# Optimization experiments

Hardware: AMD Instinct MI355X
Metric: run time of the kernel (lower is better)

## Reference

```python
import jax, jax.numpy as jnp
import numpy as np

N_NODES = 50000
N_EDGES = 800000
IN_CH = 128
OUT_CH = 64
HID = 2 * OUT_CH  # 128
NEG_SLOPE = 0.2  # PyG GATConv default negative_slope


def gat_conv(x, edge_index, W, a_src, a_dst, b):
    """Single-head PyG GATConv (heads=1, concat=True, self-loops already in edge_index)."""
    N = x.shape[0]
    h = x @ W  # [N, C]
    src, dst = edge_index[0], edge_index[1]
    # per-edge attention logits: leaky_relu(a_src . h_src + a_dst . h_dst)
    e = jax.nn.leaky_relu((h @ a_src)[src] + (h @ a_dst)[dst], NEG_SLOPE)  # [E]
    # softmax over incoming edges of each dst node (numerically stable)
    m = jax.ops.segment_max(e, dst, num_segments=N)
    p = jnp.exp(e - m[dst])
    denom = jax.ops.segment_sum(p, dst, num_segments=N)
    coef = p / denom[dst]  # [E]
    # scatter-aggregate weighted source features
    out = jax.ops.segment_sum(coef[:, None] * h[src], dst, num_segments=N)  # [N, C]
    return out + b


def setup_inputs() -> dict:
    key = jax.random.key(0)
    ks = jax.random.split(key, 12)
    s_in = 1.0 / np.sqrt(IN_CH)
    s_h = 1.0 / np.sqrt(HID)
    return {
        "x": jax.random.normal(ks[0], (N_NODES, IN_CH), dtype=jnp.float32),
        "edge_index": jax.random.randint(ks[1], (2, N_EDGES), 0, N_NODES, dtype=jnp.int64),
        "W1": jax.random.normal(ks[2], (IN_CH, HID), dtype=jnp.float32) * s_in,
        "a_src1": jax.random.normal(ks[3], (HID,), dtype=jnp.float32) * s_h,
        "a_dst1": jax.random.normal(ks[4], (HID,), dtype=jnp.float32) * s_h,
        "b1": jnp.zeros((HID,), dtype=jnp.float32),
        "W_mu": jax.random.normal(ks[5], (HID, OUT_CH), dtype=jnp.float32) * s_h,
        "a_src_mu": jax.random.normal(ks[6], (OUT_CH,), dtype=jnp.float32) * 0.125,
        "a_dst_mu": jax.random.normal(ks[7], (OUT_CH,), dtype=jnp.float32) * 0.125,
        "b_mu": jnp.zeros((OUT_CH,), dtype=jnp.float32),
        "W_ls": jax.random.normal(ks[8], (HID, OUT_CH), dtype=jnp.float32) * s_h,
        "a_src_ls": jax.random.normal(ks[9], (OUT_CH,), dtype=jnp.float32) * 0.125,
        "a_dst_ls": jax.random.normal(ks[10], (OUT_CH,), dtype=jnp.float32) * 0.125,
        "b_ls": jnp.zeros((OUT_CH,), dtype=jnp.float32),
    }


def reference(x, edge_index, W1, a_src1, a_dst1, b1, W_mu, a_src_mu, a_dst_mu, b_mu, W_ls, a_src_ls, a_dst_ls, b_ls):
    N = x.shape[0]
    loops = jnp.arange(N, dtype=edge_index.dtype)
    ei = jnp.concatenate([edge_index, jnp.stack([loops, loops])], axis=1)  # add self-loops
    h = jax.nn.relu(gat_conv(x, ei, W1, a_src1, a_dst1, b1))
    mu = gat_conv(h, ei, W_mu, a_src_mu, a_dst_mu, b_mu)
    logstd = gat_conv(h, ei, W_ls, a_src_ls, a_dst_ls, b_ls)
    return mu, logstd
```

## Files before the change

### kernel.cpp

```cpp
#include <hip/hip_runtime.h>
#include <hip/hip_bf16.h>
#include <math.h>

typedef __attribute__((ext_vector_type(8))) _Float16 half8;
typedef __attribute__((ext_vector_type(4))) float f32x4;


__device__ __forceinline__ float leaky02(float v) { return v > 0.0f ? v : 0.2f * v; }

__device__ __forceinline__ unsigned short f2bf(float f) {
  unsigned u = __float_as_uint(f);
  u += 0x7FFF + ((u >> 16) & 1);
  return (unsigned short)(u >> 16);
}
__device__ __forceinline__ float2 bfp(unsigned v) {
  float2 r;
  r.x = __uint_as_float(v << 16);
  r.y = __uint_as_float(v & 0xFFFF0000u);
  return r;
}


#define BSHIFT 9
#define BDSTS 512

__global__ __launch_bounds__(256) void bucket_hist_kernel(
    const int* __restrict__ ei, int* __restrict__ bcount, int E, int NBUCK) {
  __shared__ int h[128];
  if (threadIdx.x < 128) h[threadIdx.x] = 0;
  __syncthreads();
  for (int e = blockIdx.x * blockDim.x + threadIdx.x; e < E; e += gridDim.x * blockDim.x)
    atomicAdd(&h[ei[E + e] >> BSHIFT], 1);
  __syncthreads();
  if (threadIdx.x < NBUCK && h[threadIdx.x]) atomicAdd(&bcount[threadIdx.x], h[threadIdx.x]);
}

__global__ __launch_bounds__(128) void bucket_scan_kernel(
    const int* __restrict__ bcount, int* __restrict__ bstart, int* __restrict__ bcursor,
    int* __restrict__ row_start, int NBUCK, int E, int N) {
  __shared__ int lds[128];
  int t = threadIdx.x;
  int v = (t < NBUCK) ? bcount[t] : 0;
  lds[t] = v;
  __syncthreads();
#pragma unroll
  for (int off = 1; off < 128; off <<= 1) {
    int tmp = (t >= off) ? lds[t - off] : 0;
    __syncthreads();
    lds[t] += tmp;
    __syncthreads();
  }
  if (t < NBUCK) {
    int excl = lds[t] - v;
    bstart[t] = excl;
    bcursor[t] = excl;
  }
  if (t == 0) { bstart[NBUCK] = E; row_start[N] = E; }
}

#define CHUNK 4096
__global__ __launch_bounds__(256) void pair_scatter_kernel(
    const int* __restrict__ ei, int* __restrict__ bcursor, unsigned* __restrict__ pairs, int E) {
  __shared__ int h[128], base[128], cur[128];
  if (threadIdx.x < 128) { h[threadIdx.x] = 0; cur[threadIdx.x] = 0; }
  __syncthreads();
  int c0 = blockIdx.x * CHUNK;
  int c1 = min(c0 + CHUNK, E);
  for (int e = c0 + (int)threadIdx.x; e < c1; e += 256)
    atomicAdd(&h[ei[E + e] >> BSHIFT], 1);
  __syncthreads();
  if (threadIdx.x < 128 && h[threadIdx.x])
    base[threadIdx.x] = atomicAdd(&bcursor[threadIdx.x], h[threadIdx.x]);
  __syncthreads();
  for (int e = c0 + (int)threadIdx.x; e < c1; e += 256) {
    int dst = ei[E + e];
    int src = ei[e];
    int b = dst >> BSHIFT;
    int r = atomicAdd(&cur[b], 1);
    pairs[base[b] + r] = ((unsigned)src << BSHIFT) | (unsigned)(dst & (BDSTS - 1));
  }
}

__global__ __launch_bounds__(512) void fine_kernel(
    const unsigned* __restrict__ pairs, const int* __restrict__ bstart,
    int* __restrict__ row_start, int* __restrict__ esrc, int N) {
  __shared__ int h[BDSTS], sc[BDSTS], cur[BDSTS];
  int t = threadIdx.x;
  int b = blockIdx.x;
  int d0 = b << BSHIFT;
  int d1 = min(d0 + BDSTS, N);
  int beg = bstart[b], end = bstart[b + 1];
  h[t] = 0;
  __syncthreads();
  for (int i = beg + t; i < end; i += 512) atomicAdd(&h[pairs[i] & (BDSTS - 1)], 1);
  __syncthreads();
  int v = h[t];
  sc[t] = v;
  __syncthreads();
#pragma unroll
  for (int off = 1; off < BDSTS; off <<= 1) {
    int tmp = (t >= off) ? sc[t - off] : 0;
    __syncthreads();
    sc[t] += tmp;
    __syncthreads();
  }
  int excl = sc[t] - v;
  if (d0 + t < d1) row_start[d0 + t] = beg + excl;
  cur[t] = excl;
  __syncthreads();
  for (int i = beg + t; i < end; i += 512) {
    unsigned p = pairs[i];
    int r = atomicAdd(&cur[p & (BDSTS - 1)], 1);
    esrc[beg + r] = (int)(p >> BSHIFT);
  }
}


__global__ __launch_bounds__(256) void prep_w_kernel(
    const float* __restrict__ W1, const float* __restrict__ Wmu, const float* __restrict__ Wls,
    _Float16* __restrict__ Wt1, _Float16* __restrict__ Wt2) {
  int idx = blockIdx.x * 256 + threadIdx.x;
  int c = idx >> 7, k = idx & 127;
  Wt1[idx] = (_Float16)W1[k * 128 + c];
  float w2 = (c < 64) ? Wmu[k * 64 + c] : Wls[k * 64 + (c - 64)];
  Wt2[idx] = (_Float16)w2;
}


__global__ __launch_bounds__(256) void gemm1_mfma(
    const float* __restrict__ X, const _Float16* __restrict__ Wt,
    const float* __restrict__ a_src, const float* __restrict__ a_dst,
    unsigned short* __restrict__ Hb, float* __restrict__ asrc, float* __restrict__ adst, int N) {
  const int wid = threadIdx.x >> 6, lane = threadIdx.x & 63;
  const int r16 = (blockIdx.x * 4 + wid) * 16;
  if (r16 >= N) return;
  const int cg = lane & 15;
  const int kq = (lane >> 4) * 8;
  const int rA = r16 + cg;
  const int rowClamp = min(rA, N - 1);

  f32x4 acc[8];
#pragma unroll
  for (int j = 0; j < 8; ++j) acc[j] = (f32x4){0.f, 0.f, 0.f, 0.f};

#pragma unroll
  for (int ks = 0; ks < 4; ++ks) {
    const int k0 = ks * 32;
    const float* xp = X + (size_t)rowClamp * 128 + k0 + kq;
    float4 xa = *(const float4*)xp;
    float4 xb = *(const float4*)(xp + 4);
    half8 a;
    a[0] = (_Float16)xa.x; a[1] = (_Float16)xa.y; a[2] = (_Float16)xa.z; a[3] = (_Float16)xa.w;
    a[4] = (_Float16)xb.x; a[5] = (_Float16)xb.y; a[6] = (_Float16)xb.z; a[7] = (_Float16)xb.w;
#pragma unroll
    for (int j = 0; j < 8; ++j) {
      half8 b = *(const half8*)(Wt + (size_t)(16 * j + cg) * 128 + k0 + kq);
      acc[j] = __builtin_amdgcn_mfma_f32_16x16x32_f16(a, b, acc[j], 0, 0, 0);
    }
  }

  float as_[8], ds_[8];
#pragma unroll
  for (int j = 0; j < 8; ++j) { as_[j] = a_src[16 * j + cg]; ds_[j] = a_dst[16 * j + cg]; }
  const int rg = (lane >> 4) * 4;
#pragma unroll
  for (int reg = 0; reg < 4; ++reg) {
    int row = r16 + rg + reg;
    bool ok = row < N;
    float ps = 0.f, pd = 0.f;
#pragma unroll
    for (int j = 0; j < 8; ++j) {
      float v = acc[j][reg];
      if (ok) Hb[(size_t)row * 128 + 16 * j + cg] = f2bf(v);
      ps = fmaf(v, as_[j], ps);
      pd = fmaf(v, ds_[j], pd);
    }
#pragma unroll
    for (int o = 1; o < 16; o <<= 1) { ps += __shfl_xor(ps, o); pd += __shfl_xor(pd, o); }
    if (ok && cg == 0) { asrc[row] = ps; adst[row] = pd; }
  }
}

__global__ __launch_bounds__(256) void gemm2_mfma(
    const _Float16* __restrict__ Xh, const _Float16* __restrict__ Wt,
    const float* __restrict__ a_src_mu, const float* __restrict__ a_dst_mu,
    const float* __restrict__ a_src_ls, const float* __restrict__ a_dst_ls,
    unsigned short* __restrict__ Hb, float* __restrict__ as2, float* __restrict__ ad2, int N) {
  const int wid = threadIdx.x >> 6, lane = threadIdx.x & 63;
  const int r16 = (blockIdx.x * 4 + wid) * 16;
  if (r16 >= N) return;
  const int cg = lane & 15;
  const int kq = (lane >> 4) * 8;
  const int rA = r16 + cg;
  const int rowClamp = min(rA, N - 1);

  f32x4 acc[8];
#pragma unroll
  for (int j = 0; j < 8; ++j) acc[j] = (f32x4){0.f, 0.f, 0.f, 0.f};

#pragma unroll
  for (int ks = 0; ks < 4; ++ks) {
    const int k0 = ks * 32;
    half8 a = *(const half8*)(Xh + (size_t)rowClamp * 128 + k0 + kq);
#pragma unroll
    for (int j = 0; j < 8; ++j) {
      half8 b = *(const half8*)(Wt + (size_t)(16 * j + cg) * 128 + k0 + kq);
      acc[j] = __builtin_amdgcn_mfma_f32_16x16x32_f16(a, b, acc[j], 0, 0, 0);
    }
  }

  float asv[8], adv[8];
#pragma unroll
  for (int j = 0; j < 4; ++j) {
    asv[j] = a_src_mu[16 * j + cg]; adv[j] = a_dst_mu[16 * j + cg];
    asv[j + 4] = a_src_ls[16 * j + cg]; adv[j + 4] = a_dst_ls[16 * j + cg];
  }
  const int rg = (lane >> 4) * 4;
#pragma unroll
  for (int reg = 0; reg < 4; ++reg) {
    int row = r16 + rg + reg;
    bool ok = row < N;
    float psm = 0.f, pdm = 0.f, psl = 0.f, pdl = 0.f;
#pragma unroll
    for (int j = 0; j < 8; ++j) {
      float v = acc[j][reg];
      if (ok) Hb[(size_t)row * 128 + 16 * j + cg] = f2bf(v);
      if (j < 4) { psm = fmaf(v, asv[j], psm); pdm = fmaf(v, adv[j], pdm); }
      else       { psl = fmaf(v, asv[j], psl); pdl = fmaf(v, adv[j], pdl); }
    }
#pragma unroll
    for (int o = 1; o < 16; o <<= 1) {
      psm += __shfl_xor(psm, o); pdm += __shfl_xor(pdm, o);
      psl += __shfl_xor(psl, o); pdl += __shfl_xor(pdl, o);
    }
    if (ok && cg == 0) {
      as2[2 * row] = psm; ad2[2 * row] = pdm;
      as2[2 * row + 1] = psl; ad2[2 * row + 1] = pdl;
    }
  }
}


__global__ __launch_bounds__(256) void agg1_pv(
    const unsigned short* __restrict__ Hb, const float* __restrict__ asrc,
    const float* __restrict__ adst, const int* __restrict__ row_start,
    const int* __restrict__ esrc, const float* __restrict__ b,
    _Float16* __restrict__ hout, int N) {
  const int lane = threadIdx.x & 63;
  const int half = lane >> 5, sub = lane & 31;
  const int g = (int)(blockIdx.x * 4 + (threadIdx.x >> 6));
  const int d = g * 2 + half;
  const bool dok = d < N;
  const int dc = dok ? d : N - 1;
  const float ad = adst[dc];
  float m = leaky02(asrc[dc] + ad);
  float den = 1.0f;
  uint2 sv = *(const uint2*)(Hb + (size_t)dc * 128 + sub * 4);
  float2 f0 = bfp(sv.x), f1 = bfp(sv.y);
  float a0 = f0.x, a1 = f0.y, a2 = f1.x, a3 = f1.y;
  const int beg = row_start[dc];
  const int n = dok ? (row_start[dc + 1] - beg) : 0;
  int nmax = n;
#pragma unroll
  for (int o = 32; o > 0; o >>= 1) nmax = max(nmax, __shfl_xor(nmax, o));
  const int hbase = half * 32;
  for (int c0 = 0; c0 < nmax; c0 += 32) {
    int j = c0 + sub;
    bool v = j < n;
    int s = v ? esrc[beg + j] : dc;
    float e = v ? leaky02(asrc[s] + ad) : -INFINITY;
    float cm = e;
#pragma unroll
    for (int o = 16; o > 0; o >>= 1) cm = fmaxf(cm, __shfl_xor(cm, o));
    float mn = fmaxf(m, cm);
    float sc = __expf(m - mn);
    m = mn;
    den *= sc; a0 *= sc; a1 *= sc; a2 *= sc; a3 *= sc;
    float w = __expf(e - m);
    float ws = w;
#pragma unroll
    for (int o = 16; o > 0; o >>= 1) ws += __shfl_xor(ws, o);
    den += ws;
    int cnt = n - c0; if (cnt > 32) cnt = 32;
    int jj = 0;
    for (; jj + 4 <= cnt; jj += 4) {
      int s0 = __shfl(s, hbase + jj), s1 = __shfl(s, hbase + jj + 1);
      int s2 = __shfl(s, hbase + jj + 2), s3 = __shfl(s, hbase + jj + 3);
      float w0 = __shfl(w, hbase + jj), w1 = __shfl(w, hbase + jj + 1);
      float w2 = __shfl(w, hbase + jj + 2), w3 = __shfl(w, hbase + jj + 3);
      uint2 h0 = *(const uint2*)(Hb + (size_t)s0 * 128 + sub * 4);
      uint2 h1 = *(const uint2*)(Hb + (size_t)s1 * 128 + sub * 4);
      uint2 h2 = *(const uint2*)(Hb + (size_t)s2 * 128 + sub * 4);
      uint2 h3 = *(const uint2*)(Hb + (size_t)s3 * 128 + sub * 4);
      float2 p0 = bfp(h0.x), p1 = bfp(h0.y);
      a0 = fmaf(w0, p0.x, a0); a1 = fmaf(w0, p0.y, a1); a2 = fmaf(w0, p1.x, a2); a3 = fmaf(w0, p1.y, a3);
      p0 = bfp(h1.x); p1 = bfp(h1.y);
      a0 = fmaf(w1, p0.x, a0); a1 = fmaf(w1, p0.y, a1); a2 = fmaf(w1, p1.x, a2); a3 = fmaf(w1, p1.y, a3);
      p0 = bfp(h2.x); p1 = bfp(h2.y);
      a0 = fmaf(w2, p0.x, a0); a1 = fmaf(w2, p0.y, a1); a2 = fmaf(w2, p1.x, a2); a3 = fmaf(w2, p1.y, a3);
      p0 = bfp(h3.x); p1 = bfp(h3.y);
      a0 = fmaf(w3, p0.x, a0); a1 = fmaf(w3, p0.y, a1); a2 = fmaf(w3, p1.x, a2); a3 = fmaf(w3, p1.y, a3);
    }
    for (; jj < cnt; ++jj) {
      int sj = __shfl(s, hbase + jj);
      float wj = __shfl(w, hbase + jj);
      uint2 hv = *(const uint2*)(Hb + (size_t)sj * 128 + sub * 4);
      float2 p0 = bfp(hv.x), p1 = bfp(hv.y);
      a0 = fmaf(wj, p0.x, a0); a1 = fmaf(wj, p0.y, a1);
      a2 = fmaf(wj, p1.x, a2); a3 = fmaf(wj, p1.y, a3);
    }
  }
  if (dok) {
    float inv = 1.0f / den;
    float4 bv = *(const float4*)(b + sub * 4);
    _Float16 o4[4];
    o4[0] = (_Float16)fmaxf(fmaf(a0, inv, bv.x), 0.f);
    o4[1] = (_Float16)fmaxf(fmaf(a1, inv, bv.y), 0.f);
    o4[2] = (_Float16)fmaxf(fmaf(a2, inv, bv.z), 0.f);
    o4[3] = (_Float16)fmaxf(fmaf(a3, inv, bv.w), 0.f);
    *(uint2*)(hout + (size_t)d * 128 + sub * 4) = *(uint2*)o4;
  }
}


__global__ __launch_bounds__(256) void agg2_pv(
    const unsigned short* __restrict__ Hb,
    const float2* __restrict__ as2, const float2* __restrict__ ad2,
    const int* __restrict__ row_start, const int* __restrict__ esrc,
    const float* __restrict__ b_mu, const float* __restrict__ b_ls,
    float* __restrict__ out_mu, float* __restrict__ out_ls, int N) {
  const int lane = threadIdx.x & 63;
  const int half = lane >> 5, sub = lane & 31;
  const bool isMu = sub < 16;
  const int g = (int)(blockIdx.x * 4 + (threadIdx.x >> 6));
  const int d = g * 2 + half;
  const bool dok = d < N;
  const int dc = dok ? d : N - 1;
  const float2 adv = ad2[dc];
  const float2 asv = as2[dc];
  float mm = leaky02(asv.x + adv.x);
  float ml = leaky02(asv.y + adv.y);
  float den_m = 1.0f, den_l = 1.0f;
  uint2 sv = *(const uint2*)(Hb + (size_t)dc * 128 + sub * 4);
  float2 f0 = bfp(sv.x), f1 = bfp(sv.y);
  float a0 = f0.x, a1 = f0.y, a2 = f1.x, a3 = f1.y;
  const int beg = row_start[dc];
  const int n = dok ? (row_start[dc + 1] - beg) : 0;
  int nmax = n;
#pragma unroll
  for (int o = 32; o > 0; o >>= 1) nmax = max(nmax, __shfl_xor(nmax, o));
  const int hbase = half * 32;
  for (int c0 = 0; c0 < nmax; c0 += 32) {
    int j = c0 + sub;
    bool v = j < n;
    int s = v ? esrc[beg + j] : dc;
    float em = -INFINITY, el = -INFINITY;
    if (v) {
      float2 av = as2[s];
      em = leaky02(av.x + adv.x);
      el = leaky02(av.y + adv.y);
    }
    float cmm = em, cml = el;
#pragma unroll
    for (int o = 16; o > 0; o >>= 1) {
      cmm = fmaxf(cmm, __shfl_xor(cmm, o));
      cml = fmaxf(cml, __shfl_xor(cml, o));
    }
    float mnm = fmaxf(mm, cmm), mnl = fmaxf(ml, cml);
    float scm = __expf(mm - mnm), scl = __expf(ml - mnl);
    mm = mnm; ml = mnl;
    den_m *= scm; den_l *= scl;
    float sce = isMu ? scm : scl;
    a0 *= sce; a1 *= sce; a2 *= sce; a3 *= sce;
    float wm = __expf(em - mm), wl = __expf(el - ml);
    float wsm = wm, wsl = wl;
#pragma unroll
    for (int o = 16; o > 0; o >>= 1) {
      wsm += __shfl_xor(wsm, o);
      wsl += __shfl_xor(wsl, o);
    }
    den_m += wsm; den_l += wsl;
    int cnt = n - c0; if (cnt > 32) cnt = 32;
    int jj = 0;
    for (; jj + 4 <= cnt; jj += 4) {
      int s0 = __shfl(s, hbase + jj), s1 = __shfl(s, hbase + jj + 1);
      int s2 = __shfl(s, hbase + jj + 2), s3 = __shfl(s, hbase + jj + 3);
      float wm0 = __shfl(wm, hbase + jj), wm1 = __shfl(wm, hbase + jj + 1);
      float wm2 = __shfl(wm, hbase + jj + 2), wm3 = __shfl(wm, hbase + jj + 3);
      float wl0 = __shfl(wl, hbase + jj), wl1 = __shfl(wl, hbase + jj + 1);
      float wl2 = __shfl(wl, hbase + jj + 2), wl3 = __shfl(wl, hbase + jj + 3);
      float w0 = isMu ? wm0 : wl0, w1 = isMu ? wm1 : wl1;
      float w2 = isMu ? wm2 : wl2, w3 = isMu ? wm3 : wl3;
      uint2 h0 = *(const uint2*)(Hb + (size_t)s0 * 128 + sub * 4);
      uint2 h1 = *(const uint2*)(Hb + (size_t)s1 * 128 + sub * 4);
      uint2 h2 = *(const uint2*)(Hb + (size_t)s2 * 128 + sub * 4);
      uint2 h3 = *(const uint2*)(Hb + (size_t)s3 * 128 + sub * 4);
      float2 p0 = bfp(h0.x), p1 = bfp(h0.y);
      a0 = fmaf(w0, p0.x, a0); a1 = fmaf(w0, p0.y, a1); a2 = fmaf(w0, p1.x, a2); a3 = fmaf(w0, p1.y, a3);
      p0 = bfp(h1.x); p1 = bfp(h1.y);
      a0 = fmaf(w1, p0.x, a0); a1 = fmaf(w1, p0.y, a1); a2 = fmaf(w1, p1.x, a2); a3 = fmaf(w1, p1.y, a3);
      p0 = bfp(h2.x); p1 = bfp(h2.y);
      a0 = fmaf(w2, p0.x, a0); a1 = fmaf(w2, p0.y, a1); a2 = fmaf(w2, p1.x, a2); a3 = fmaf(w2, p1.y, a3);
      p0 = bfp(h3.x); p1 = bfp(h3.y);
      a0 = fmaf(w3, p0.x, a0); a1 = fmaf(w3, p0.y, a1); a2 = fmaf(w3, p1.x, a2); a3 = fmaf(w3, p1.y, a3);
    }
    for (; jj < cnt; ++jj) {
      int sj = __shfl(s, hbase + jj);
      float wmj = __shfl(wm, hbase + jj);
      float wlj = __shfl(wl, hbase + jj);
      float wj = isMu ? wmj : wlj;
      uint2 hv = *(const uint2*)(Hb + (size_t)sj * 128 + sub * 4);
      float2 p0 = bfp(hv.x), p1 = bfp(hv.y);
      a0 = fmaf(wj, p0.x, a0); a1 = fmaf(wj, p0.y, a1);
      a2 = fmaf(wj, p1.x, a2); a3 = fmaf(wj, p1.y, a3);
    }
  }
  if (dok) {
    float inv = isMu ? (1.0f / den_m) : (1.0f / den_l);
    const float* bp;
    float* op;
    if (isMu) { bp = b_mu + sub * 4; op = out_mu + (size_t)d * 64 + sub * 4; }
    else      { bp = b_ls + sub * 4 - 64; op = out_ls + (size_t)d * 64 + sub * 4 - 64; }
    float4 bv = *(const float4*)bp;
    float4 o;
    o.x = fmaf(a0, inv, bv.x);
    o.y = fmaf(a1, inv, bv.y);
    o.z = fmaf(a2, inv, bv.z);
    o.w = fmaf(a3, inv, bv.w);
    *(float4*)op = o;
  }
}


extern "C" void kernel_launch(void* const* d_in, const int* in_sizes, int n_in,
                              void* d_out, int out_size, void* d_ws, size_t ws_size,
                              hipStream_t stream) {
  const float* x = (const float*)d_in[0];
  const int* ei = (const int*)d_in[1];
  const float* W1 = (const float*)d_in[2];
  const float* a_src1 = (const float*)d_in[3];
  const float* a_dst1 = (const float*)d_in[4];
  const float* b1 = (const float*)d_in[5];
  const float* W_mu = (const float*)d_in[6];
  const float* a_src_mu = (const float*)d_in[7];
  const float* a_dst_mu = (const float*)d_in[8];
  const float* b_mu = (const float*)d_in[9];
  const float* W_ls = (const float*)d_in[10];
  const float* a_src_ls = (const float*)d_in[11];
  const float* a_dst_ls = (const float*)d_in[12];
  const float* b_ls = (const float*)d_in[13];

  const int N = in_sizes[0] / 128;
  const int E = in_sizes[1] / 2;
  const int NBUCK = (N + BDSTS - 1) >> BSHIFT;

  uint8_t* p = (uint8_t*)d_ws;
  auto carve = [&](size_t bytes) -> void* {
    void* q = (void*)p;
    p += (bytes + 255) & ~(size_t)255;
    return q;
  };
  int* bcount = (int*)carve((size_t)(NBUCK + 1) * 4);
  int* bstart = (int*)carve((size_t)(NBUCK + 1) * 4);
  int* bcursor = (int*)carve((size_t)NBUCK * 4);
  int* row_start = (int*)carve((size_t)(N + 1) * 4);
  int* esrc = (int*)carve((size_t)E * 4);
  unsigned* pairs = (unsigned*)carve((size_t)E * 4);
  unsigned short* Hb1 = (unsigned short*)carve((size_t)N * 128 * 2);
  _Float16* h1 = (_Float16*)carve((size_t)N * 128 * 2);
  _Float16* Wt1 = (_Float16*)carve((size_t)128 * 128 * 2);
  _Float16* Wt2 = (_Float16*)carve((size_t)128 * 128 * 2);
  float* as1 = (float*)carve((size_t)N * 4);
  float* ad1 = (float*)carve((size_t)N * 4);
  float* as2 = (float*)carve((size_t)N * 8);
  float* ad2 = (float*)carve((size_t)N * 8);

  unsigned short* Hb2 = Hb1;

  hipMemsetAsync(bcount, 0, (size_t)(NBUCK + 1) * 4, stream);
  prep_w_kernel<<<64, 256, 0, stream>>>(W1, W_mu, W_ls, Wt1, Wt2);
  bucket_hist_kernel<<<(E + 2047) / 2048, 256, 0, stream>>>(ei, bcount, E, NBUCK);
  bucket_scan_kernel<<<1, 128, 0, stream>>>(bcount, bstart, bcursor, row_start, NBUCK, E, N);
  pair_scatter_kernel<<<(E + CHUNK - 1) / CHUNK, 256, 0, stream>>>(ei, bcursor, pairs, E);
  fine_kernel<<<NBUCK, 512, 0, stream>>>(pairs, bstart, row_start, esrc, N);

  gemm1_mfma<<<(N + 63) / 64, 256, 0, stream>>>(x, Wt1, a_src1, a_dst1, Hb1, as1, ad1, N);
  const int nwaves = (N + 1) / 2;
  const int nblk = (nwaves + 3) / 4;
  agg1_pv<<<nblk, 256, 0, stream>>>(Hb1, as1, ad1, row_start, esrc, b1, h1, N);
  gemm2_mfma<<<(N + 63) / 64, 256, 0, stream>>>(h1, Wt2, a_src_mu, a_dst_mu,
                                                a_src_ls, a_dst_ls, Hb2, as2, ad2, N);
  float* out_mu = (float*)d_out;
  float* out_ls = out_mu + (size_t)N * 64;
  agg2_pv<<<nblk, 256, 0, stream>>>(Hb2, (const float2*)as2, (const float2*)ad2,
                                    row_start, esrc, b_mu, b_ls, out_mu, out_ls, N);
}
```

Measured before the change: 165.6 us.

## Drop online-max softmax, fuse bucket histogram into gemm1, shrink buckets

The aggregation kernels drop the numerically stable online-max softmax. They compute exp(leaky(e)) directly, accumulate per-lane denominators, and reduce once at the end, which removes the per-chunk max/sum shuffles and rescaling. The gather loop is unrolled to 8 edges per iteration. The bucket histogram is merged into the gemm1 launch as extra blocks, and the bucket size is halved to 256 destinations so fine_kernel runs 256-thread blocks. Skipping the max subtraction risks exp overflow for large logits, and the NBUCK buffer size must match the new bucket count (256 is needed for 50000 nodes).

```diff
diff --git a/kernel.cpp b/kernel.cpp
--- a/kernel.cpp
+++ b/kernel.cpp
@@ -21,30 +21,19 @@
 }
 
 
-#define BSHIFT 9
-#define BDSTS 512
-
-__global__ __launch_bounds__(256) void bucket_hist_kernel(
-    const int* __restrict__ ei, int* __restrict__ bcount, int E, int NBUCK) {
-  __shared__ int h[128];
-  if (threadIdx.x < 128) h[threadIdx.x] = 0;
-  __syncthreads();
-  for (int e = blockIdx.x * blockDim.x + threadIdx.x; e < E; e += gridDim.x * blockDim.x)
-    atomicAdd(&h[ei[E + e] >> BSHIFT], 1);
-  __syncthreads();
-  if (threadIdx.x < NBUCK && h[threadIdx.x]) atomicAdd(&bcount[threadIdx.x], h[threadIdx.x]);
-}
-
-__global__ __launch_bounds__(128) void bucket_scan_kernel(
+#define BSHIFT 8
+#define BDSTS 256
+
+__global__ __launch_bounds__(256) void bucket_scan_kernel(
     const int* __restrict__ bcount, int* __restrict__ bstart, int* __restrict__ bcursor,
     int* __restrict__ row_start, int NBUCK, int E, int N) {
-  __shared__ int lds[128];
+  __shared__ int lds[256];
   int t = threadIdx.x;
   int v = (t < NBUCK) ? bcount[t] : 0;
   lds[t] = v;
   __syncthreads();
 #pragma unroll
-  for (int off = 1; off < 128; off <<= 1) {
+  for (int off = 1; off < 256; off <<= 1) {
     int tmp = (t >= off) ? lds[t - off] : 0;
     __syncthreads();
     lds[t] += tmp;
@@ -61,15 +50,15 @@
 #define CHUNK 4096
 __global__ __launch_bounds__(256) void pair_scatter_kernel(
     const int* __restrict__ ei, int* __restrict__ bcursor, unsigned* __restrict__ pairs, int E) {
-  __shared__ int h[128], base[128], cur[128];
-  if (threadIdx.x < 128) { h[threadIdx.x] = 0; cur[threadIdx.x] = 0; }
+  __shared__ int h[256], base[256], cur[256];
+  h[threadIdx.x] = 0; cur[threadIdx.x] = 0;
   __syncthreads();
   int c0 = blockIdx.x * CHUNK;
   int c1 = min(c0 + CHUNK, E);
   for (int e = c0 + (int)threadIdx.x; e < c1; e += 256)
     atomicAdd(&h[ei[E + e] >> BSHIFT], 1);
   __syncthreads();
-  if (threadIdx.x < 128 && h[threadIdx.x])
+  if (h[threadIdx.x])
     base[threadIdx.x] = atomicAdd(&bcursor[threadIdx.x], h[threadIdx.x]);
   __syncthreads();
   for (int e = c0 + (int)threadIdx.x; e < c1; e += 256) {
@@ -81,18 +70,17 @@
   }
 }
 
-__global__ __launch_bounds__(512) void fine_kernel(
+__global__ __launch_bounds__(256) void fine_kernel(
     const unsigned* __restrict__ pairs, const int* __restrict__ bstart,
     int* __restrict__ row_start, int* __restrict__ esrc, int N) {
   __shared__ int h[BDSTS], sc[BDSTS], cur[BDSTS];
   int t = threadIdx.x;
   int b = blockIdx.x;
   int d0 = b << BSHIFT;
-  int d1 = min(d0 + BDSTS, N);
   int beg = bstart[b], end = bstart[b + 1];
   h[t] = 0;
   __syncthreads();
-  for (int i = beg + t; i < end; i += 512) atomicAdd(&h[pairs[i] & (BDSTS - 1)], 1);
+  for (int i = beg + t; i < end; i += 256) atomicAdd(&h[pairs[i] & (BDSTS - 1)], 1);
   __syncthreads();
   int v = h[t];
   sc[t] = v;
@@ -105,10 +93,10 @@
     __syncthreads();
   }
   int excl = sc[t] - v;
-  if (d0 + t < d1) row_start[d0 + t] = beg + excl;
+  if (d0 + t < N) row_start[d0 + t] = beg + excl;
   cur[t] = excl;
   __syncthreads();
-  for (int i = beg + t; i < end; i += 512) {
+  for (int i = beg + t; i < end; i += 256) {
     unsigned p = pairs[i];
     int r = atomicAdd(&cur[p & (BDSTS - 1)], 1);
     esrc[beg + r] = (int)(p >> BSHIFT);
@@ -127,12 +115,26 @@
 }
 
 
-__global__ __launch_bounds__(256) void gemm1_mfma(
+__global__ __launch_bounds__(256) void gemm1_hist(
     const float* __restrict__ X, const _Float16* __restrict__ Wt,
     const float* __restrict__ a_src, const float* __restrict__ a_dst,
-    unsigned short* __restrict__ Hb, float* __restrict__ asrc, float* __restrict__ adst, int N) {
+    unsigned short* __restrict__ Hb, float* __restrict__ asrc, float* __restrict__ adst, int N,
+    const int* __restrict__ ei, int* __restrict__ bcount, int E, int nGB) {
+  if ((int)blockIdx.x >= nGB) {
+    __shared__ int h[256];
+    h[threadIdx.x] = 0;
+    __syncthreads();
+    int hb = (int)blockIdx.x - nGB;
+    int c0 = hb * 2048;
+    int c1 = min(c0 + 2048, E);
+    for (int e = c0 + (int)threadIdx.x; e < c1; e += 256)
+      atomicAdd(&h[ei[E + e] >> BSHIFT], 1);
+    __syncthreads();
+    if (h[threadIdx.x]) atomicAdd(&bcount[threadIdx.x], h[threadIdx.x]);
+    return;
+  }
   const int wid = threadIdx.x >> 6, lane = threadIdx.x & 63;
-  const int r16 = (blockIdx.x * 4 + wid) * 16;
+  const int r16 = ((int)blockIdx.x * 4 + wid) * 16;
   if (r16 >= N) return;
   const int cg = lane & 15;
   const int kq = (lane >> 4) * 8;
@@ -187,7 +189,7 @@
     const float* __restrict__ a_src_ls, const float* __restrict__ a_dst_ls,
     unsigned short* __restrict__ Hb, float* __restrict__ as2, float* __restrict__ ad2, int N) {
   const int wid = threadIdx.x >> 6, lane = threadIdx.x & 63;
-  const int r16 = (blockIdx.x * 4 + wid) * 16;
+  const int r16 = ((int)blockIdx.x * 4 + wid) * 16;
   if (r16 >= N) return;
   const int cg = lane & 15;
   const int kq = (lane >> 4) * 8;
@@ -241,7 +243,17 @@
 }
 
 
-__global__ __launch_bounds__(256) void agg1_pv(
+#define GATH(K)                                                          \
+  {                                                                      \
+    int sA = __shfl(s, hbase + jj + K);                                  \
+    float wA = __shfl(w, hbase + jj + K);                                \
+    uint2 hA = *(const uint2*)(Hb + (size_t)sA * 128 + sub * 4);         \
+    float2 pa = bfp(hA.x), pb = bfp(hA.y);                               \
+    a0 = fmaf(wA, pa.x, a0); a1 = fmaf(wA, pa.y, a1);                    \
+    a2 = fmaf(wA, pb.x, a2); a3 = fmaf(wA, pb.y, a3);                    \
+  }
+
+__global__ __launch_bounds__(256) void agg1_ns(
     const unsigned short* __restrict__ Hb, const float* __restrict__ asrc,
     const float* __restrict__ adst, const int* __restrict__ row_start,
     const int* __restrict__ esrc, const float* __restrict__ b,
@@ -253,63 +265,33 @@
   const bool dok = d < N;
   const int dc = dok ? d : N - 1;
   const float ad = adst[dc];
-  float m = leaky02(asrc[dc] + ad);
-  float den = 1.0f;
+  const float wself = __expf(leaky02(asrc[dc] + ad));
   uint2 sv = *(const uint2*)(Hb + (size_t)dc * 128 + sub * 4);
   float2 f0 = bfp(sv.x), f1 = bfp(sv.y);
-  float a0 = f0.x, a1 = f0.y, a2 = f1.x, a3 = f1.y;
+  float a0 = wself * f0.x, a1 = wself * f0.y, a2 = wself * f1.x, a3 = wself * f1.y;
+  float den = (sub == 0) ? wself : 0.f;
   const int beg = row_start[dc];
   const int n = dok ? (row_start[dc + 1] - beg) : 0;
-  int nmax = n;
-#pragma unroll
-  for (int o = 32; o > 0; o >>= 1) nmax = max(nmax, __shfl_xor(nmax, o));
+  const int nmax = max(n, __shfl_xor(n, 32));
   const int hbase = half * 32;
   for (int c0 = 0; c0 < nmax; c0 += 32) {
     int j = c0 + sub;
     bool v = j < n;
-    int s = v ? esrc[beg + j] : dc;
-    float e = v ? leaky02(asrc[s] + ad) : -INFINITY;
-    float cm = e;
-#pragma unroll
-    for (int o = 16; o > 0; o >>= 1) cm = fmaxf(cm, __shfl_xor(cm, o));
-    float mn = fmaxf(m, cm);
-    float sc = __expf(m - mn);
-    m = mn;
-    den *= sc; a0 *= sc; a1 *= sc; a2 *= sc; a3 *= sc;
-    float w = __expf(e - m);
-    float ws = w;
-#pragma unroll
-    for (int o = 16; o > 0; o >>= 1) ws += __shfl_xor(ws, o);
-    den += ws;
-    int cnt = n - c0; if (cnt > 32) cnt = 32;
+    int s = v ? esrc[beg + j] : 0;
+    float w = 0.f;
+    if (v) w = __expf(leaky02(asrc[s] + ad));
+    den += w;
+    int cnt = n - c0;
+    if (cnt > 32) cnt = 32;
+    if (cnt < 0) cnt = 0;
     int jj = 0;
-    for (; jj + 4 <= cnt; jj += 4) {
-      int s0 = __shfl(s, hbase + jj), s1 = __shfl(s, hbase + jj + 1);
-      int s2 = __shfl(s, hbase + jj + 2), s3 = __shfl(s, hbase + jj + 3);
-      float w0 = __shfl(w, hbase + jj), w1 = __shfl(w, hbase + jj + 1);
-      float w2 = __shfl(w, hbase + jj + 2), w3 = __shfl(w, hbase + jj + 3);
-      uint2 h0 = *(const uint2*)(Hb + (size_t)s0 * 128 + sub * 4);
-      uint2 h1 = *(const uint2*)(Hb + (size_t)s1 * 128 + sub * 4);
-      uint2 h2 = *(const uint2*)(Hb + (size_t)s2 * 128 + sub * 4);
-      uint2 h3 = *(const uint2*)(Hb + (size_t)s3 * 128 + sub * 4);
-      float2 p0 = bfp(h0.x), p1 = bfp(h0.y);
-      a0 = fmaf(w0, p0.x, a0); a1 = fmaf(w0, p0.y, a1); a2 = fmaf(w0, p1.x, a2); a3 = fmaf(w0, p1.y, a3);
-      p0 = bfp(h1.x); p1 = bfp(h1.y);
-      a0 = fmaf(w1, p0.x, a0); a1 = fmaf(w1, p0.y, a1); a2 = fmaf(w1, p1.x, a2); a3 = fmaf(w1, p1.y, a3);
-      p0 = bfp(h2.x); p1 = bfp(h2.y);
-      a0 = fmaf(w2, p0.x, a0); a1 = fmaf(w2, p0.y, a1); a2 = fmaf(w2, p1.x, a2); a3 = fmaf(w2, p1.y, a3);
-      p0 = bfp(h3.x); p1 = bfp(h3.y);
-      a0 = fmaf(w3, p0.x, a0); a1 = fmaf(w3, p0.y, a1); a2 = fmaf(w3, p1.x, a2); a3 = fmaf(w3, p1.y, a3);
-    }
-    for (; jj < cnt; ++jj) {
-      int sj = __shfl(s, hbase + jj);
-      float wj = __shfl(w, hbase + jj);
-      uint2 hv = *(const uint2*)(Hb + (size_t)sj * 128 + sub * 4);
-      float2 p0 = bfp(hv.x), p1 = bfp(hv.y);
-      a0 = fmaf(wj, p0.x, a0); a1 = fmaf(wj, p0.y, a1);
-      a2 = fmaf(wj, p1.x, a2); a3 = fmaf(wj, p1.y, a3);
-    }
-  }
+    for (; jj + 8 <= cnt; jj += 8) {
+      GATH(0) GATH(1) GATH(2) GATH(3) GATH(4) GATH(5) GATH(6) GATH(7)
+    }
+    for (; jj < cnt; ++jj) GATH(0)
+  }
+#pragma unroll
+  for (int o = 16; o > 0; o >>= 1) den += __shfl_xor(den, o);
   if (dok) {
     float inv = 1.0f / den;
     float4 bv = *(const float4*)(b + sub * 4);
@@ -323,7 +305,19 @@
 }
 
 
-__global__ __launch_bounds__(256) void agg2_pv(
+#define GATH2(K)                                                         \
+  {                                                                      \
+    int sA = __shfl(s, hbase + jj + K);                                  \
+    float wmA = __shfl(wm, hbase + jj + K);                              \
+    float wlA = __shfl(wl, hbase + jj + K);                              \
+    float wA = isMu ? wmA : wlA;                                         \
+    uint2 hA = *(const uint2*)(Hb + (size_t)sA * 128 + sub * 4);         \
+    float2 pa = bfp(hA.x), pb = bfp(hA.y);                               \
+    a0 = fmaf(wA, pa.x, a0); a1 = fmaf(wA, pa.y, a1);                    \
+    a2 = fmaf(wA, pb.x, a2); a3 = fmaf(wA, pb.y, a3);                    \
+  }
+
+__global__ __launch_bounds__(256) void agg2_ns(
     const unsigned short* __restrict__ Hb,
     const float2* __restrict__ as2, const float2* __restrict__ ad2,
     const int* __restrict__ row_start, const int* __restrict__ esrc,
@@ -338,82 +332,43 @@
   const int dc = dok ? d : N - 1;
   const float2 adv = ad2[dc];
   const float2 asv = as2[dc];
-  float mm = leaky02(asv.x + adv.x);
-  float ml = leaky02(asv.y + adv.y);
-  float den_m = 1.0f, den_l = 1.0f;
+  const float wself_m = __expf(leaky02(asv.x + adv.x));
+  const float wself_l = __expf(leaky02(asv.y + adv.y));
   uint2 sv = *(const uint2*)(Hb + (size_t)dc * 128 + sub * 4);
   float2 f0 = bfp(sv.x), f1 = bfp(sv.y);
-  float a0 = f0.x, a1 = f0.y, a2 = f1.x, a3 = f1.y;
+  const float wself = isMu ? wself_m : wself_l;
+  float a0 = wself * f0.x, a1 = wself * f0.y, a2 = wself * f1.x, a3 = wself * f1.y;
+  float den_m = (sub == 0) ? wself_m : 0.f;
+  float den_l = (sub == 0) ? wself_l : 0.f;
   const int beg = row_start[dc];
   const int n = dok ? (row_start[dc + 1] - beg) : 0;
-  int nmax = n;
-#pragma unroll
-  for (int o = 32; o > 0; o >>= 1) nmax = max(nmax, __shfl_xor(nmax, o));
+  const int nmax = max(n, __shfl_xor(n, 32));
   const int hbase = half * 32;
   for (int c0 = 0; c0 < nmax; c0 += 32) {
     int j = c0 + sub;
     bool v = j < n;
-    int s = v ? esrc[beg + j] : dc;
-    float em = -INFINITY, el = -INFINITY;
+    int s = v ? esrc[beg + j] : 0;
+    float wm = 0.f, wl = 0.f;
     if (v) {
       float2 av = as2[s];
-      em = leaky02(av.x + adv.x);
-      el = leaky02(av.y + adv.y);
-    }
-    float cmm = em, cml = el;
-#pragma unroll
-    for (int o = 16; o > 0; o >>= 1) {
-      cmm = fmaxf(cmm, __shfl_xor(cmm, o));
-      cml = fmaxf(cml, __shfl_xor(cml, o));
-    }
-    float mnm = fmaxf(mm, cmm), mnl = fmaxf(ml, cml);
-    float scm = __expf(mm - mnm), scl = __expf(ml - mnl);
-    mm = mnm; ml = mnl;
-    den_m *= scm; den_l *= scl;
-    float sce = isMu ? scm : scl;
-    a0 *= sce; a1 *= sce; a2 *= sce; a3 *= sce;
-    float wm = __expf(em - mm), wl = __expf(el - ml);
-    float wsm = wm, wsl = wl;
-#pragma unroll
-    for (int o = 16; o > 0; o >>= 1) {
-      wsm += __shfl_xor(wsm, o);
-      wsl += __shfl_xor(wsl, o);
-    }
-    den_m += wsm; den_l += wsl;
-    int cnt = n - c0; if (cnt > 32) cnt = 32;
+      wm = __expf(leaky02(av.x + adv.x));
+      wl = __expf(leaky02(av.y + adv.y));
+    }
+    den_m += wm;
+    den_l += wl;
+    int cnt = n - c0;
+    if (cnt > 32) cnt = 32;
+    if (cnt < 0) cnt = 0;
     int jj = 0;
-    for (; jj + 4 <= cnt; jj += 4) {
-      int s0 = __shfl(s, hbase + jj), s1 = __shfl(s, hbase + jj + 1);
-      int s2 = __shfl(s, hbase + jj + 2), s3 = __shfl(s, hbase + jj + 3);
-      float wm0 = __shfl(wm, hbase + jj), wm1 = __shfl(wm, hbase + jj + 1);
-      float wm2 = __shfl(wm, hbase + jj + 2), wm3 = __shfl(wm, hbase + jj + 3);
-      float wl0 = __shfl(wl, hbase + jj), wl1 = __shfl(wl, hbase + jj + 1);
-      float wl2 = __shfl(wl, hbase + jj + 2), wl3 = __shfl(wl, hbase + jj + 3);
-      float w0 = isMu ? wm0 : wl0, w1 = isMu ? wm1 : wl1;
-      float w2 = isMu ? wm2 : wl2, w3 = isMu ? wm3 : wl3;
-      uint2 h0 = *(const uint2*)(Hb + (size_t)s0 * 128 + sub * 4);
-      uint2 h1 = *(const uint2*)(Hb + (size_t)s1 * 128 + sub * 4);
-      uint2 h2 = *(const uint2*)(Hb + (size_t)s2 * 128 + sub * 4);
-      uint2 h3 = *(const uint2*)(Hb + (size_t)s3 * 128 + sub * 4);
-      float2 p0 = bfp(h0.x), p1 = bfp(h0.y);
-      a0 = fmaf(w0, p0.x, a0); a1 = fmaf(w0, p0.y, a1); a2 = fmaf(w0, p1.x, a2); a3 = fmaf(w0, p1.y, a3);
-      p0 = bfp(h1.x); p1 = bfp(h1.y);
-      a0 = fmaf(w1, p0.x, a0); a1 = fmaf(w1, p0.y, a1); a2 = fmaf(w1, p1.x, a2); a3 = fmaf(w1, p1.y, a3);
-      p0 = bfp(h2.x); p1 = bfp(h2.y);
-      a0 = fmaf(w2, p0.x, a0); a1 = fmaf(w2, p0.y, a1); a2 = fmaf(w2, p1.x, a2); a3 = fmaf(w2, p1.y, a3);
-      p0 = bfp(h3.x); p1 = bfp(h3.y);
-      a0 = fmaf(w3, p0.x, a0); a1 = fmaf(w3, p0.y, a1); a2 = fmaf(w3, p1.x, a2); a3 = fmaf(w3, p1.y, a3);
-    }
-    for (; jj < cnt; ++jj) {
-      int sj = __shfl(s, hbase + jj);
-      float wmj = __shfl(wm, hbase + jj);
-      float wlj = __shfl(wl, hbase + jj);
-      float wj = isMu ? wmj : wlj;
-      uint2 hv = *(const uint2*)(Hb + (size_t)sj * 128 + sub * 4);
-      float2 p0 = bfp(hv.x), p1 = bfp(hv.y);
-      a0 = fmaf(wj, p0.x, a0); a1 = fmaf(wj, p0.y, a1);
-      a2 = fmaf(wj, p1.x, a2); a3 = fmaf(wj, p1.y, a3);
-    }
+    for (; jj + 8 <= cnt; jj += 8) {
+      GATH2(0) GATH2(1) GATH2(2) GATH2(3) GATH2(4) GATH2(5) GATH2(6) GATH2(7)
+    }
+    for (; jj < cnt; ++jj) GATH2(0)
+  }
+#pragma unroll
+  for (int o = 16; o > 0; o >>= 1) {
+    den_m += __shfl_xor(den_m, o);
+    den_l += __shfl_xor(den_l, o);
   }
   if (dok) {
     float inv = isMu ? (1.0f / den_m) : (1.0f / den_l);
@@ -479,19 +434,22 @@
 
   hipMemsetAsync(bcount, 0, (size_t)(NBUCK + 1) * 4, stream);
   prep_w_kernel<<<64, 256, 0, stream>>>(W1, W_mu, W_ls, Wt1, Wt2);
-  bucket_hist_kernel<<<(E + 2047) / 2048, 256, 0, stream>>>(ei, bcount, E, NBUCK);
-  bucket_scan_kernel<<<1, 128, 0, stream>>>(bcount, bstart, bcursor, row_start, NBUCK, E, N);
+
+  const int nGB = (N + 63) / 64;
+  const int nHB = (E + 2047) / 2048;
+  gemm1_hist<<<nGB + nHB, 256, 0, stream>>>(x, Wt1, a_src1, a_dst1, Hb1, as1, ad1, N,
+                                            ei, bcount, E, nGB);
+  bucket_scan_kernel<<<1, 256, 0, stream>>>(bcount, bstart, bcursor, row_start, NBUCK, E, N);
   pair_scatter_kernel<<<(E + CHUNK - 1) / CHUNK, 256, 0, stream>>>(ei, bcursor, pairs, E);
-  fine_kernel<<<NBUCK, 512, 0, stream>>>(pairs, bstart, row_start, esrc, N);
-
-  gemm1_mfma<<<(N + 63) / 64, 256, 0, stream>>>(x, Wt1, a_src1, a_dst1, Hb1, as1, ad1, N);
+  fine_kernel<<<NBUCK, 256, 0, stream>>>(pairs, bstart, row_start, esrc, N);
+
   const int nwaves = (N + 1) / 2;
   const int nblk = (nwaves + 3) / 4;
-  agg1_pv<<<nblk, 256, 0, stream>>>(Hb1, as1, ad1, row_start, esrc, b1, h1, N);
+  agg1_ns<<<nblk, 256, 0, stream>>>(Hb1, as1, ad1, row_start, esrc, b1, h1, N);
   gemm2_mfma<<<(N + 63) / 64, 256, 0, stream>>>(h1, Wt2, a_src_mu, a_dst_mu,
                                                 a_src_ls, a_dst_ls, Hb2, as2, ad2, N);
   float* out_mu = (float*)d_out;
   float* out_ls = out_mu + (size_t)N * 64;
-  agg2_pv<<<nblk, 256, 0, stream>>>(Hb2, (const float2*)as2, (const float2*)ad2,
+  agg2_ns<<<nblk, 256, 0, stream>>>(Hb2, (const float2*)as2, (const float2*)ad2,
                                     row_start, esrc, b_mu, b_ls, out_mu, out_ls, N);
 }
```

Measured after the change: 163.4 us. Within noise of the previous version (-1.3%).
